# Kernel optimization log

Hardware: AMD Instinct MI355X
Metric: run time of the kernel (lower is better)

## Reference

```python
import jax, jax.numpy as jnp
from jax import lax
import numpy as np

# NOTE: the original module calls an opaque CUDA 'approximate dot-product' conv kernel.
# Its backward uses EXACT conv2d gradients for input/weight, so the reference forward
# math is the exact conv2d the kernel approximates. `approximate` is a learned scalar
# controlling the hardware approximation level; it does not change the exact-math output.

STRIDE = 1
PAD = (1, 1)  # (padH, padW)


def setup_inputs() -> dict:
    key = jax.random.key(0)
    k1, k2, k3 = jax.random.split(key, 3)
    B, Cin, H, W = 32, 128, 56, 56
    Cout, K = 256, 3
    x = jax.random.normal(k1, (B, Cin, H, W), dtype=jnp.float32)
    # weight init: uniform(-1, 1) per reset_parameters
    weight = jax.random.uniform(k2, (Cout, Cin, K, K), dtype=jnp.float32, minval=-1.0, maxval=1.0)
    fan_in = Cin * K * K
    bound = 1.0 / np.sqrt(fan_in)
    bias = jax.random.uniform(k3, (Cout,), dtype=jnp.float32, minval=-bound, maxval=bound)
    approximate = jnp.ones((1,), dtype=jnp.float32)
    return {"x": x, "weight": weight, "bias": bias, "approximate": approximate}


def reference(x, weight, bias, approximate):
    # Exact conv2d, NCHW input, OIHW kernel. `approximate` controls only the
    # hardware approximation level in the original CUDA kernel.
    out = lax.conv_general_dilated(
        x, weight,
        window_strides=(STRIDE, STRIDE),
        padding=((PAD[0], PAD[0]), (PAD[1], PAD[1])),
        dimension_numbers=("NCHW", "OIHW", "NCHW"),
    )
    return out + bias.reshape(1, -1, 1, 1)
```

## Files before the change

kernel.cpp:

```cpp
#include <hip/hip_runtime.h>


typedef __attribute__((ext_vector_type(8))) short short8;
typedef __attribute__((ext_vector_type(4))) float floatx4;

typedef __attribute__((address_space(1))) const void* gas_ptr;
typedef __attribute__((address_space(3))) void* las_ptr;

__device__ static inline void gl2lds16(const void* g, void* l) {
    __builtin_amdgcn_global_load_lds((gas_ptr)g, (las_ptr)l, 16, 0, 0);
}

__device__ static inline float bf2f(unsigned short u) {
    union { unsigned int i; float f; } x; x.i = ((unsigned int)u) << 16; return x.f;
}
__device__ static inline unsigned short f2bf(float f) {
    union { float f; unsigned int i; } x; x.f = f;
    unsigned int r = (x.i + 0x7FFFu + ((x.i >> 16) & 1u)) >> 16;
    return (unsigned short)r;
}

__device__ static inline bool wave_detect_bf16(const unsigned int* __restrict__ p) {
    const int lane = threadIdx.x & 63;
    int cnt = 0;
#pragma unroll
    for (int r = 0; r < 4; ++r) {
        unsigned int w = p[r * 64 + lane];
        unsigned short lo = (unsigned short)(w & 0xFFFFu);
        int e = (lo >> 7) & 0xFF;
        bool plaus = (lo == 0) || (e >= 96 && e <= 144);
        cnt += (int)__popcll(__ballot(plaus));
    }
    return cnt >= 205;
}

__global__ void wt_repack(const void* __restrict__ wsrc,
                          unsigned short* __restrict__ wt) {
    const bool isbf = wave_detect_bf16((const unsigned int*)wsrc);
    int idx  = blockIdx.x * 256 + threadIdx.x;
    int lane = idx & 63;
    int i    = (idx >> 6) & 7;
    int wm   = (idx >> 9) & 1;
    int q    = (idx >> 10) & 3;
    int off  = idx >> 12;
    int co   = wm * 128 + i * 16 + (lane & 15);
    int ci0  = q * 32 + (lane >> 4) * 8;
    union { unsigned short s[8]; uint4 u; } pk;
#pragma unroll
    for (int e = 0; e < 8; ++e) {
        size_t s = (size_t)(co * 128 + ci0 + e) * 9 + off;
        float v = isbf ? bf2f(((const unsigned short*)wsrc)[s])
                       : ((const float*)wsrc)[s];
        pk.s[e] = f2bf(v);
    }
    *(uint4*)(wt + (size_t)idx * 8) = pk.u;
}

__global__ __launch_bounds__(256) void x_repack(
    const void* __restrict__ xsrc, unsigned short* __restrict__ xp) {
    __shared__ unsigned short tile[56 * 130];
    const int bh  = blockIdx.x;
    const int b   = bh / 58, hp = bh - b * 58;
    const int tid = threadIdx.x;
    unsigned short* row = xp + (size_t)(b * 58 + hp) * 58 * 128;
    if (hp == 0 || hp == 57) {
        uint4 z; z.x = z.y = z.z = z.w = 0u;
        uint4* r = (uint4*)row;
        for (int t = tid; t < 928; t += 256) r[t] = z;
        return;
    }
    const bool isbf = wave_detect_bf16((const unsigned int*)xsrc);
    const int h = hp - 1;
    if (isbf) {
        const unsigned short* xs =
            (const unsigned short*)xsrc + (size_t)b * 128 * 3136 + h * 56;
#pragma unroll
        for (int it = 0; it < 7; ++it) {
            int idx = it * 256 + tid;
            int ci = idx / 14, w4 = idx - ci * 14;
            ushort4 v = *(const ushort4*)(xs + (size_t)ci * 3136 + w4 * 4);
            tile[(w4 * 4 + 0) * 130 + ci] = v.x;
            tile[(w4 * 4 + 1) * 130 + ci] = v.y;
            tile[(w4 * 4 + 2) * 130 + ci] = v.z;
            tile[(w4 * 4 + 3) * 130 + ci] = v.w;
        }
    } else {
        const float* xs = (const float*)xsrc + (size_t)b * 128 * 3136 + h * 56;
#pragma unroll
        for (int it = 0; it < 7; ++it) {
            int idx = it * 256 + tid;
            int ci = idx / 14, w4 = idx - ci * 14;
            float4 v = *(const float4*)(xs + (size_t)ci * 3136 + w4 * 4);
            tile[(w4 * 4 + 0) * 130 + ci] = f2bf(v.x);
            tile[(w4 * 4 + 1) * 130 + ci] = f2bf(v.y);
            tile[(w4 * 4 + 2) * 130 + ci] = f2bf(v.z);
            tile[(w4 * 4 + 3) * 130 + ci] = f2bf(v.w);
        }
    }
    __syncthreads();
#pragma unroll
    for (int it = 0; it < 4; ++it) {
        int k = it * 256 + tid;
        if (k >= 928) break;
        int wq = k >> 4, cc = k & 15;
        uint4 v;
        if (wq == 0 || wq == 57) { v.x = v.y = v.z = v.w = 0u; }
        else {
            const unsigned short* p = &tile[(wq - 1) * 130 + cc * 8];
            union { unsigned short s[8]; uint4 u; } pk;
#pragma unroll
            for (int j = 0; j < 8; ++j) pk.s[j] = p[j];
            v = pk.u;
        }
        *(uint4*)(row + wq * 128 + cc * 8) = v;
    }
}

__global__ __launch_bounds__(256, 2) void conv_mfma(
    const unsigned short* __restrict__ xp,
    const unsigned short* __restrict__ wt,
    const void* __restrict__ bias,
    void* __restrict__ out,
    const void* __restrict__ xorig)
{
    __shared__ __align__(16) char lds[16384];
    const int tid   = threadIdx.x;
    const int lane  = tid & 63;
    const int wv    = tid >> 6;
    const int bid   = blockIdx.x;
    const int ntile = (bid & 7) * 98 + (bid >> 3);

    const bool isbf = wave_detect_bf16((const unsigned int*)xorig);

    const int clg  = (lane & 3) ^ ((lane >> 3) & 3);
    const int rsub = lane >> 2;
    unsigned sbB[2]; int dbB[2];
#pragma unroll
    for (int s = 0; s < 2; ++s) {
        const int c = wv * 2 + s;
        const int n = ntile * 128 + c * 16 + rsub;
        const int b = n / 3136, rem = n - b * 3136;
        const int hh = rem / 56, ww = rem - hh * 56;
        sbB[s] = (unsigned)(((b * 58 + hh) * 58 + ww) * 256 + clg * 16);
        dbB[s] = c * 1024;
    }

    const int fr = lane & 15;
    const int ph = (lane >> 4) ^ ((fr >> 1) & 3);
    const int wm = wv >> 1;
    const int wn = wv & 1;
    const int bOff = (wn * 64 + fr) * 64 + ph * 16;
    const int aSub = wm * 4096 + lane * 8;

    floatx4 acc[8][4] = {};
    short8 afA[8], afB[8];

#pragma unroll
    for (int i_ = 0; i_ < 8; ++i_)
        afA[i_] = *(const short8*)(wt + aSub + i_ * 512);
    gl2lds16((const char*)xp + sbB[0], lds + dbB[0]);
    gl2lds16((const char*)xp + sbB[1], lds + dbB[1]);
    __builtin_amdgcn_s_waitcnt(0x3F70);
    __builtin_amdgcn_s_barrier();

#define BODY(H, AF_USE, AF_LOAD)                                           \
  {                                                                        \
    {                                                                      \
      const unsigned short* aP = wt + (size_t)((H) + 1) * 8192 + aSub;     \
      _Pragma("unroll")                                                    \
      for (int i_ = 0; i_ < 8; ++i_)                                       \
        AF_LOAD[i_] = *(const short8*)(aP + i_ * 512);                     \
    }                                                                      \
    {                                                                      \
      char* sd = lds + (((H) + 1) & 1) * 8192;                             \
      const int hn = (H) + 1, off_ = hn >> 2, qq = hn & 3;                 \
      const int dh_ = off_ / 3, dw_ = off_ - dh_ * 3;                      \
      const int dB = (dh_ * 58 + dw_) * 256 + qq * 64;                     \
      gl2lds16((const char*)xp + sbB[0] + dB, sd + dbB[0]);                \
      gl2lds16((const char*)xp + sbB[1] + dB, sd + dbB[1]);                \
    }                                                                      \
    short8 bfr[4];                                                         \
    {                                                                      \
      const char* la = lds + ((H) & 1) * 8192;                             \
      bfr[0] = *(const short8*)(la + bOff);                                \
      bfr[1] = *(const short8*)(la + bOff + 1024);                         \
      bfr[2] = *(const short8*)(la + bOff + 2048);                         \
      bfr[3] = *(const short8*)(la + bOff + 3072);                         \
    }                                                                      \
    __builtin_amdgcn_s_setprio(1);                                         \
    _Pragma("unroll")                                                      \
    for (int i_ = 0; i_ < 8; ++i_) {                                       \
      _Pragma("unroll")                                                    \
      for (int j_ = 0; j_ < 4; ++j_)                                       \
        acc[i_][j_] = __builtin_amdgcn_mfma_f32_16x16x32_bf16(             \
            AF_USE[i_], bfr[j_], acc[i_][j_], 0, 0, 0);                    \
    }                                                                      \
    __builtin_amdgcn_s_setprio(0);                                         \
    __builtin_amdgcn_s_waitcnt(0x3F70);                                    \
    __builtin_amdgcn_s_barrier();                                          \
  }

    for (int h = 0; h < 34; h += 2) {
        BODY(h,     afA, afB);
        BODY(h + 1, afB, afA);
    }
    BODY(34, afA, afB);
    {
        const char* la = lds + 8192;
        short8 bfr[4];
        bfr[0] = *(const short8*)(la + bOff);
        bfr[1] = *(const short8*)(la + bOff + 1024);
        bfr[2] = *(const short8*)(la + bOff + 2048);
        bfr[3] = *(const short8*)(la + bOff + 3072);
#pragma unroll
        for (int i_ = 0; i_ < 8; ++i_)
#pragma unroll
            for (int j_ = 0; j_ < 4; ++j_)
                acc[i_][j_] = __builtin_amdgcn_mfma_f32_16x16x32_bf16(
                    afB[i_], bfr[j_], acc[i_][j_], 0, 0, 0);
    }

    const int q4 = (lane >> 4) << 2;
    int nb[4], ns[4];
#pragma unroll
    for (int j = 0; j < 4; ++j) {
        const int n = ntile * 128 + wn * 64 + j * 16 + fr;
        nb[j] = n / 3136;
        ns[j] = n - nb[j] * 3136;
    }
#pragma unroll
    for (int i = 0; i < 8; ++i) {
        const int co = wm * 128 + i * 16 + q4;
        float bv[4];
        if (isbf) {
            const ushort4 bb = *(const ushort4*)((const unsigned short*)bias + co);
            bv[0] = bf2f(bb.x); bv[1] = bf2f(bb.y);
            bv[2] = bf2f(bb.z); bv[3] = bf2f(bb.w);
        } else {
            const float4 bb = *(const float4*)((const float*)bias + co);
            bv[0] = bb.x; bv[1] = bb.y; bv[2] = bb.z; bv[3] = bb.w;
        }
#pragma unroll
        for (int j = 0; j < 4; ++j) {
#pragma unroll
            for (int r = 0; r < 4; ++r) {
                const float v = acc[i][j][r] + bv[r];
                const size_t o = (size_t)nb[j] * 802816 +
                                 (size_t)(co + r) * 3136 + ns[j];
                if (isbf) ((unsigned short*)out)[o] = f2bf(v);
                else      ((float*)out)[o] = v;
            }
        }
    }
}

__global__ void conv_naive(const float* __restrict__ x,
                           const float* __restrict__ w,
                           const float* __restrict__ bias,
                           float* __restrict__ out) {
    long long i = (long long)blockIdx.x * 256 + threadIdx.x;
    if (i >= 25690112LL) return;
    int wo = (int)(i % 56); long long t = i / 56;
    int ho = (int)(t % 56); t /= 56;
    int co = (int)(t % 256); int b = (int)(t / 256);
    float acc = bias[co];
    for (int ci = 0; ci < 128; ++ci)
        for (int dh = 0; dh < 3; ++dh) {
            int hi = ho + dh - 1; if ((unsigned)hi >= 56u) continue;
            for (int dw = 0; dw < 3; ++dw) {
                int wi = wo + dw - 1; if ((unsigned)wi >= 56u) continue;
                acc += x[((size_t)(b * 128 + ci) * 56 + hi) * 56 + wi] *
                       w[((co * 128 + ci) * 3 + dh) * 3 + dw];
            }
        }
    out[i] = acc;
}

extern "C" void kernel_launch(void* const* d_in, const int* in_sizes, int n_in,
                              void* d_out, int out_size, void* d_ws, size_t ws_size,
                              hipStream_t stream) {
    const void* x    = d_in[0];
    const void* w    = d_in[1];
    const void* bias = d_in[2];

    const size_t xp_bytes = (size_t)32 * 58 * 58 * 128 * 2;
    const size_t wt_off   = xp_bytes;
    const size_t wt_bytes = (size_t)9 * 256 * 128 * 2;
    const size_t need     = wt_off + wt_bytes;

    if (ws_size >= need) {
        unsigned short* xp = (unsigned short*)d_ws;
        unsigned short* wt = (unsigned short*)((char*)d_ws + wt_off);
        x_repack<<<32 * 58, 256, 0, stream>>>(x, xp);
        wt_repack<<<144, 256, 0, stream>>>(w, wt);
        conv_mfma<<<dim3(784, 1, 1), 256, 0, stream>>>(xp, wt, bias, d_out, x);
    } else {
        conv_naive<<<(25690112 + 255) / 256, 256, 0, stream>>>(
            (const float*)x, (const float*)w, (const float*)bias, (float*)d_out);
    }
}
```

Before: 212.1 us.

## Load conv input fragments directly from global into registers, drop LDS staging

Removes the LDS double buffer, the global_load_lds transfers and the per-step barriers. Each wave now loads its B (input) fragments straight from global memory into registers with double buffering, as it already does for weights. The aim is to cut barrier and LDS round-trip overhead. In exchange, each input element is fetched by both wm waves instead of once per block, which raises global/L2 traffic and register pressure.

```diff
diff --git a/kernel.cpp b/kernel.cpp
--- a/kernel.cpp
+++ b/kernel.cpp
@@ -3,13 +3,6 @@
 
 typedef __attribute__((ext_vector_type(8))) short short8;
 typedef __attribute__((ext_vector_type(4))) float floatx4;
-
-typedef __attribute__((address_space(1))) const void* gas_ptr;
-typedef __attribute__((address_space(3))) void* las_ptr;
-
-__device__ static inline void gl2lds16(const void* g, void* l) {
-    __builtin_amdgcn_global_load_lds((gas_ptr)g, (las_ptr)l, 16, 0, 0);
-}
 
 __device__ static inline float bf2f(unsigned short u) {
     union { unsigned int i; float f; } x; x.i = ((unsigned int)u) << 16; return x.f;
@@ -123,7 +116,6 @@
     void* __restrict__ out,
     const void* __restrict__ xorig)
 {
-    __shared__ __align__(16) char lds[16384];
     const int tid   = threadIdx.x;
     const int lane  = tid & 63;
     const int wv    = tid >> 6;
@@ -132,95 +124,70 @@
 
     const bool isbf = wave_detect_bf16((const unsigned int*)xorig);
 
-    const int clg  = (lane & 3) ^ ((lane >> 3) & 3);
-    const int rsub = lane >> 2;
-    unsigned sbB[2]; int dbB[2];
-#pragma unroll
-    for (int s = 0; s < 2; ++s) {
-        const int c = wv * 2 + s;
-        const int n = ntile * 128 + c * 16 + rsub;
+    const int fr = lane & 15;
+    const int hi = lane >> 4;
+    const int wm = wv >> 1;
+    const int wn = wv & 1;
+
+    const unsigned short* aP = wt + (wm * 4096 + lane * 8);
+
+    const unsigned short* bP[4];
+#pragma unroll
+    for (int j = 0; j < 4; ++j) {
+        const int n = ntile * 128 + wn * 64 + j * 16 + fr;
         const int b = n / 3136, rem = n - b * 3136;
         const int hh = rem / 56, ww = rem - hh * 56;
-        sbB[s] = (unsigned)(((b * 58 + hh) * 58 + ww) * 256 + clg * 16);
-        dbB[s] = c * 1024;
-    }
-
-    const int fr = lane & 15;
-    const int ph = (lane >> 4) ^ ((fr >> 1) & 3);
-    const int wm = wv >> 1;
-    const int wn = wv & 1;
-    const int bOff = (wn * 64 + fr) * 64 + ph * 16;
-    const int aSub = wm * 4096 + lane * 8;
+        bP[j] = xp + (size_t)((b * 58 + hh) * 58 + ww) * 128 + hi * 8;
+    }
 
     floatx4 acc[8][4] = {};
-    short8 afA[8], afB[8];
-
-#pragma unroll
-    for (int i_ = 0; i_ < 8; ++i_)
-        afA[i_] = *(const short8*)(wt + aSub + i_ * 512);
-    gl2lds16((const char*)xp + sbB[0], lds + dbB[0]);
-    gl2lds16((const char*)xp + sbB[1], lds + dbB[1]);
-    __builtin_amdgcn_s_waitcnt(0x3F70);
-    __builtin_amdgcn_s_barrier();
-
-#define BODY(H, AF_USE, AF_LOAD)                                           \
+    short8 afA[8], afB[8], bfA[4], bfB[4];
+
+#pragma unroll
+    for (int j = 0; j < 4; ++j) bfA[j] = *(const short8*)(bP[j]);
+#pragma unroll
+    for (int i = 0; i < 8; ++i) afA[i] = *(const short8*)(aP + i * 512);
+
+#define BODY(H, AU, AL, BU, BL)                                            \
   {                                                                        \
+    const int hn = (H) + 1, off_ = hn >> 2, qq = hn & 3;                   \
+    const int dh_ = off_ / 3, dw_ = off_ - dh_ * 3;                        \
+    const int dB = (dh_ * 58 + dw_) * 128 + qq * 32;                       \
+    _Pragma("unroll")                                                      \
+    for (int j_ = 0; j_ < 4; ++j_)                                         \
+        BL[j_] = *(const short8*)(bP[j_] + dB);                            \
     {                                                                      \
-      const unsigned short* aP = wt + (size_t)((H) + 1) * 8192 + aSub;     \
-      _Pragma("unroll")                                                    \
-      for (int i_ = 0; i_ < 8; ++i_)                                       \
-        AF_LOAD[i_] = *(const short8*)(aP + i_ * 512);                     \
-    }                                                                      \
-    {                                                                      \
-      char* sd = lds + (((H) + 1) & 1) * 8192;                             \
-      const int hn = (H) + 1, off_ = hn >> 2, qq = hn & 3;                 \
-      const int dh_ = off_ / 3, dw_ = off_ - dh_ * 3;                      \
-      const int dB = (dh_ * 58 + dw_) * 256 + qq * 64;                     \
-      gl2lds16((const char*)xp + sbB[0] + dB, sd + dbB[0]);                \
-      gl2lds16((const char*)xp + sbB[1] + dB, sd + dbB[1]);                \
-    }                                                                      \
-    short8 bfr[4];                                                         \
-    {                                                                      \
-      const char* la = lds + ((H) & 1) * 8192;                             \
-      bfr[0] = *(const short8*)(la + bOff);                                \
-      bfr[1] = *(const short8*)(la + bOff + 1024);                         \
-      bfr[2] = *(const short8*)(la + bOff + 2048);                         \
-      bfr[3] = *(const short8*)(la + bOff + 3072);                         \
+        const unsigned short* aN = aP + (size_t)hn * 8192;                 \
+        _Pragma("unroll")                                                  \
+        for (int i_ = 0; i_ < 8; ++i_)                                     \
+            AL[i_] = *(const short8*)(aN + i_ * 512);                      \
     }                                                                      \
     __builtin_amdgcn_s_setprio(1);                                         \
     _Pragma("unroll")                                                      \
     for (int i_ = 0; i_ < 8; ++i_) {                                       \
-      _Pragma("unroll")                                                    \
-      for (int j_ = 0; j_ < 4; ++j_)                                       \
-        acc[i_][j_] = __builtin_amdgcn_mfma_f32_16x16x32_bf16(             \
-            AF_USE[i_], bfr[j_], acc[i_][j_], 0, 0, 0);                    \
+        _Pragma("unroll")                                                  \
+        for (int j_ = 0; j_ < 4; ++j_)                                     \
+            acc[i_][j_] = __builtin_amdgcn_mfma_f32_16x16x32_bf16(         \
+                AU[i_], BL == bfB ? BU[j_] : BU[j_], acc[i_][j_], 0, 0, 0);\
     }                                                                      \
     __builtin_amdgcn_s_setprio(0);                                         \
-    __builtin_amdgcn_s_waitcnt(0x3F70);                                    \
-    __builtin_amdgcn_s_barrier();                                          \
   }
 
     for (int h = 0; h < 34; h += 2) {
-        BODY(h,     afA, afB);
-        BODY(h + 1, afB, afA);
-    }
-    BODY(34, afA, afB);
-    {
-        const char* la = lds + 8192;
-        short8 bfr[4];
-        bfr[0] = *(const short8*)(la + bOff);
-        bfr[1] = *(const short8*)(la + bOff + 1024);
-        bfr[2] = *(const short8*)(la + bOff + 2048);
-        bfr[3] = *(const short8*)(la + bOff + 3072);
-#pragma unroll
-        for (int i_ = 0; i_ < 8; ++i_)
-#pragma unroll
-            for (int j_ = 0; j_ < 4; ++j_)
-                acc[i_][j_] = __builtin_amdgcn_mfma_f32_16x16x32_bf16(
-                    afB[i_], bfr[j_], acc[i_][j_], 0, 0, 0);
-    }
-
-    const int q4 = (lane >> 4) << 2;
+        BODY(h,     afA, afB, bfA, bfB);
+        BODY(h + 1, afB, afA, bfB, bfA);
+    }
+    BODY(34, afA, afB, bfA, bfB);
+    __builtin_amdgcn_s_setprio(1);
+#pragma unroll
+    for (int i_ = 0; i_ < 8; ++i_)
+#pragma unroll
+        for (int j_ = 0; j_ < 4; ++j_)
+            acc[i_][j_] = __builtin_amdgcn_mfma_f32_16x16x32_bf16(
+                afB[i_], bfB[j_], acc[i_][j_], 0, 0, 0);
+    __builtin_amdgcn_s_setprio(0);
+
+    const int q4 = hi << 2;
     int nb[4], ns[4];
 #pragma unroll
     for (int j = 0; j < 4; ++j) {
```

After: 250.5 us. 18.1% more time.

## Triple-buffer input tiles in LDS with a prefetch distance of two stages

Applied to the files above, without the earlier changes.

Grows the LDS staging area from two to three buffers and issues the global-to-LDS loads two reduction steps ahead instead of one, rotating buffer indices each step. It removes the explicit vmcnt wait before every barrier and folds the peeled final step into the main loop using guarded prefetches. The goal is to hide global load latency behind more MFMA work per barrier. The trade-off is more LDS per block. Correctness now relies on the compiler inserting waits for the asynchronous LDS DMA writes, which is a race risk.

```diff
diff --git a/kernel.cpp b/kernel.cpp
--- a/kernel.cpp
+++ b/kernel.cpp
@@ -123,7 +123,7 @@
     void* __restrict__ out,
     const void* __restrict__ xorig)
 {
-    __shared__ __align__(16) char lds[16384];
+    __shared__ __align__(16) char lds[24576];
     const int tid   = threadIdx.x;
     const int lane  = tid & 63;
     const int wv    = tid >> 6;
@@ -155,33 +155,36 @@
     floatx4 acc[8][4] = {};
     short8 afA[8], afB[8];
 
+    gl2lds16((const char*)xp + sbB[0], lds + dbB[0]);
+    gl2lds16((const char*)xp + sbB[1], lds + dbB[1]);
+    gl2lds16((const char*)xp + sbB[0] + 64, lds + 8192 + dbB[0]);
+    gl2lds16((const char*)xp + sbB[1] + 64, lds + 8192 + dbB[1]);
+    __builtin_amdgcn_sched_barrier(0);
 #pragma unroll
     for (int i_ = 0; i_ < 8; ++i_)
         afA[i_] = *(const short8*)(wt + aSub + i_ * 512);
-    gl2lds16((const char*)xp + sbB[0], lds + dbB[0]);
-    gl2lds16((const char*)xp + sbB[1], lds + dbB[1]);
-    __builtin_amdgcn_s_waitcnt(0x3F70);
-    __builtin_amdgcn_s_barrier();
+    __syncthreads();
 
 #define BODY(H, AF_USE, AF_LOAD)                                           \
   {                                                                        \
-    {                                                                      \
-      const unsigned short* aP = wt + (size_t)((H) + 1) * 8192 + aSub;     \
-      _Pragma("unroll")                                                    \
-      for (int i_ = 0; i_ < 8; ++i_)                                       \
-        AF_LOAD[i_] = *(const short8*)(aP + i_ * 512);                     \
-    }                                                                      \
-    {                                                                      \
-      char* sd = lds + (((H) + 1) & 1) * 8192;                             \
-      const int hn = (H) + 1, off_ = hn >> 2, qq = hn & 3;                 \
+    if ((H) < 34) {                                                        \
+      char* sd = lds + st_ * 8192;                                         \
+      const int hn = (H) + 2, off_ = hn >> 2, qq = hn & 3;                 \
       const int dh_ = off_ / 3, dw_ = off_ - dh_ * 3;                      \
       const int dB = (dh_ * 58 + dw_) * 256 + qq * 64;                     \
       gl2lds16((const char*)xp + sbB[0] + dB, sd + dbB[0]);                \
       gl2lds16((const char*)xp + sbB[1] + dB, sd + dbB[1]);                \
     }                                                                      \
+    __builtin_amdgcn_sched_barrier(0);                                     \
+    if ((H) < 35) {                                                        \
+      const unsigned short* aN = wt + (size_t)((H) + 1) * 8192 + aSub;     \
+      _Pragma("unroll")                                                    \
+      for (int i_ = 0; i_ < 8; ++i_)                                       \
+        AF_LOAD[i_] = *(const short8*)(aN + i_ * 512);                     \
+    }                                                                      \
     short8 bfr[4];                                                         \
     {                                                                      \
-      const char* la = lds + ((H) & 1) * 8192;                             \
+      const char* la = lds + bf_ * 8192;                                   \
       bfr[0] = *(const short8*)(la + bOff);                                \
       bfr[1] = *(const short8*)(la + bOff + 1024);                         \
       bfr[2] = *(const short8*)(la + bOff + 2048);                         \
@@ -196,28 +199,15 @@
             AF_USE[i_], bfr[j_], acc[i_][j_], 0, 0, 0);                    \
     }                                                                      \
     __builtin_amdgcn_s_setprio(0);                                         \
-    __builtin_amdgcn_s_waitcnt(0x3F70);                                    \
-    __builtin_amdgcn_s_barrier();                                          \
+    if ((H) < 35) __builtin_amdgcn_s_barrier();                            \
+    bf_ = (bf_ == 2) ? 0 : bf_ + 1;                                        \
+    st_ = (st_ == 2) ? 0 : st_ + 1;                                        \
   }
 
-    for (int h = 0; h < 34; h += 2) {
+    int bf_ = 0, st_ = 2;
+    for (int h = 0; h < 36; h += 2) {
         BODY(h,     afA, afB);
         BODY(h + 1, afB, afA);
-    }
-    BODY(34, afA, afB);
-    {
-        const char* la = lds + 8192;
-        short8 bfr[4];
-        bfr[0] = *(const short8*)(la + bOff);
-        bfr[1] = *(const short8*)(la + bOff + 1024);
-        bfr[2] = *(const short8*)(la + bOff + 2048);
-        bfr[3] = *(const short8*)(la + bOff + 3072);
-#pragma unroll
-        for (int i_ = 0; i_ < 8; ++i_)
-#pragma unroll
-            for (int j_ = 0; j_ < 4; ++j_)
-                acc[i_][j_] = __builtin_amdgcn_mfma_f32_16x16x32_bf16(
-                    afB[i_], bfr[j_], acc[i_][j_], 0, 0, 0);
     }
 
     const int q4 = (lane >> 4) << 2;
```

Measured after the change: 231.1 us. +8.9%, slower.
